# Kernel optimization log

Hardware: AMD Instinct MI355X
Metric: run time of the kernel (lower is better)

Reference implementation:

```python
import jax, jax.numpy as jnp
import numpy as np

EPS = 1e-5
K = 9  # 3x3 kernel taps


def _deform_conv_bn_relu(x, w_off, b_off, w, gamma, beta):
    B, C, H, W = x.shape
    dt = x.dtype
    # offset-predicting conv: [B, 2*K, H, W], channel layout (y,x) pairs per tap (mmcv v1)
    offset = jax.lax.conv_general_dilated(
        x, w_off, window_strides=(1, 1), padding=((1, 1), (1, 1)),
        dimension_numbers=('NCHW', 'OIHW', 'NCHW')) + b_off[None, :, None, None]
    off = offset.reshape(B, K, 2, H, W)
    # kernel tap displacements relative to output pixel (padding=1 -> centered 3x3)
    dy = (jnp.arange(K) // 3 - 1).astype(dt)
    dx = (jnp.arange(K) % 3 - 1).astype(dt)
    ii = jnp.arange(H, dtype=dt)[:, None]
    jj = jnp.arange(W, dtype=dt)[None, :]
    py = ii[None, None] + dy[None, :, None, None] + off[:, :, 0]  # [B,K,H,W]
    px = jj[None, None] + dx[None, :, None, None] + off[:, :, 1]
    y0 = jnp.floor(py)
    x0 = jnp.floor(px)
    ly = py - y0
    lx = px - x0

    xf = x.reshape(B, C, H * W)

    def gather(yc, xc, wt):
        # bilinear corner gather with zero padding outside the image
        valid = (yc >= 0) & (yc < H) & (xc >= 0) & (xc < W)
        yi = jnp.clip(yc, 0, H - 1).astype(jnp.int32)
        xi = jnp.clip(xc, 0, W - 1).astype(jnp.int32)
        idx = (yi * W + xi).reshape(B, -1)              # [B, K*H*W]
        g = jax.vmap(lambda xb, ib: xb[:, ib])(xf, idx)  # [B, C, K*H*W]
        wm = (wt * valid.astype(dt)).reshape(B, 1, -1)
        return g * wm

    val = (gather(y0, x0, (1 - ly) * (1 - lx))
           + gather(y0, x0 + 1, (1 - ly) * lx)
           + gather(y0 + 1, x0, ly * (1 - lx))
           + gather(y0 + 1, x0 + 1, ly * lx))
    val = val.reshape(B, C, K, H, W)

    # deformable conv accumulation (no bias in mmcv DeformConv2d v1)
    O = w.shape[0]
    out = jnp.einsum('ock,bckhw->bohw', w.reshape(O, C, K), val)

    # BatchNorm (training-mode batch stats) + ReLU
    mean = out.mean(axis=(0, 2, 3))
    var = out.var(axis=(0, 2, 3))
    out = (out - mean[None, :, None, None]) * jax.lax.rsqrt(var + EPS)[None, :, None, None]
    out = out * gamma[None, :, None, None] + beta[None, :, None, None]
    return jax.nn.relu(out)


def setup_inputs() -> dict:
    key = jax.random.key(0)
    k1, k2, k3 = jax.random.split(key, 3)
    B, C, O, H, W = 2, 256, 256, 128, 128
    x = jax.random.normal(k1, (B, C, H, W), dtype=jnp.float32)
    # offset branch: small init so predicted offsets stay in a realistic range
    w_off = jax.random.normal(k2, (2 * K, C, 3, 3), dtype=jnp.float32) * 0.01
    b_off = jnp.zeros((2 * K,), dtype=jnp.float32)
    w = jax.random.normal(k3, (O, C, 3, 3), dtype=jnp.float32) * 0.05
    gamma = jnp.ones((O,), dtype=jnp.float32)
    beta = jnp.zeros((O,), dtype=jnp.float32)
    return {"x": x, "w_off": w_off, "b_off": b_off, "w": w, "gamma": gamma, "beta": beta}


def reference(x, w_off, b_off, w, gamma, beta):
    return _deform_conv_bn_relu(x, w_off, b_off, w, gamma, beta)
```

## Files before the change

kernel.cpp:

```cpp
#include <hip/hip_runtime.h>
#include <hip/hip_bf16.h>

#define HWs   16384
#define Wimg  128
#define Himg  128
#define PW    130
#define PHW   16900
#define Cin   256
#define Oout  256
#define CKd   2304
#define Bb    2

typedef short   bf16x8 __attribute__((ext_vector_type(8)));
typedef float   f32x4  __attribute__((ext_vector_type(4)));

__device__ __forceinline__ float bf2f(ushort u){
  union { unsigned int i; float f; } v; v.i = ((unsigned int)u) << 16; return v.f;
}
__device__ __forceinline__ ushort f2bf(float f){
  union { float f; unsigned int i; } v; v.f = f;
  return (ushort)((v.i + 0x8000u) >> 16);
}
__device__ __forceinline__ unsigned cvt_pk_bf16(float lo, float hi){
  unsigned r;
  asm("v_cvt_pk_bf16_f32 %0, %1, %2" : "=v"(r) : "v"(lo), "v"(hi));
  return r;
}
__device__ __forceinline__ void gload_lds16(const ushort* g, void* l){
  __builtin_amdgcn_global_load_lds(
      (const __attribute__((address_space(1))) unsigned int*)g,
      (__attribute__((address_space(3))) unsigned int*)l, 16, 0, 0);
}

__global__ __launch_bounds__(256) void k_transpose(const float* __restrict__ x,
                                                   ushort* __restrict__ xtp){
  int bx = blockIdx.x;
  int b  = bx >> 10;
  int r  = bx & 1023;
  int ct = r >> 8;
  int pt = r & 255;
  int c0 = ct * 64, p0 = pt * 64;
  __shared__ float tile[64][65];
  const float* xb = x + (size_t)b * Cin * HWs;
  #pragma unroll
  for (int pass = 0; pass < 16; ++pass){
    int idx = pass * 256 + threadIdx.x;
    int cl = idx >> 6, pl = idx & 63;
    tile[cl][pl] = xb[(size_t)(c0 + cl) * HWs + p0 + pl];
  }
  __syncthreads();
  ushort* xo = xtp + (size_t)b * PHW * Cin;
  #pragma unroll
  for (int pass = 0; pass < 16; ++pass){
    int idx = pass * 256 + threadIdx.x;
    int pl = idx >> 6, cl = idx & 63;
    int hw = p0 + pl; int y = hw >> 7, xc = hw & 127;
    xo[(size_t)((y + 1) * PW + xc + 1) * Cin + c0 + cl] = f2bf(tile[cl][pl]);
  }
}

__global__ __launch_bounds__(64) void k_border(ushort* __restrict__ xtp){
  int e = blockIdx.x;
  int b = e / 516, p = e % 516;
  int y, xc;
  if (p < 130)      { y = 0;       xc = p; }
  else if (p < 260) { y = 129;     xc = p - 130; }
  else if (p < 388) { y = p - 259; xc = 0; }
  else              { y = p - 387; xc = 129; }
  uint2* dst = (uint2*)(xtp + ((size_t)b * PHW + y * PW + xc) * Cin) + threadIdx.x;
  *dst = make_uint2(0u, 0u);
}

__global__ __launch_bounds__(256) void k_wprep(const float* __restrict__ w,
                                               const float* __restrict__ wof,
                                               ushort* __restrict__ w2,
                                               ushort* __restrict__ w2of){
  int idx = blockIdx.x * 256 + threadIdx.x;
  if (idx < Oout * CKd){
    int o = idx / CKd, r = idx % CKd;
    int k = r >> 8, c = r & 255;
    w2[idx] = f2bf(w[(size_t)(o * Cin + c) * 9 + k]);
  } else {
    int j = idx - Oout * CKd;
    int o = j / CKd, r = j % CKd;
    int k = r >> 8, c = r & 255;
    float v = (o < 18) ? wof[(size_t)(o * Cin + c) * 9 + k] : 0.f;
    w2of[j] = f2bf(v);
  }
}

__global__ __launch_bounds__(512, 4) void k_offconv(const ushort* __restrict__ xtp,
                                                    const ushort* __restrict__ w2of,
                                                    const float* __restrict__ b_off,
                                                    int4* __restrict__ pidx,
                                                    float4* __restrict__ pw){
  int bx = blockIdx.x;
  int blkm = ((bx & 7) << 6) | (bx >> 3);
  int b = blkm >> 8, tile = blkm & 255;
  int hw0 = tile * 64;
  int iy = tile >> 1, jx0 = (tile & 1) * 64;
  __shared__ __align__(16) ushort aw[2][2048];
  __shared__ __align__(16) ushort bv_s[2][4096];
  __shared__ float offs_lds[18][64];
  int t = threadIdx.x, lane = t & 63, wid = t >> 6;
  int mi = wid >> 2, ni = wid & 3;
  f32x4 acc = (f32x4){0,0,0,0};
  const ushort* xb = xtp + (size_t)b * PHW * Cin;

#define OSTAGE(S, P) \
  if ((S) < 36){ int kks = (S) * 64, kt = (S) >> 2, c0s = ((S) * 64) & 255; \
    int dy = kt / 3 - 1, dxx = kt % 3 - 1; \
    if (wid < 4){ int L = t * 16; int oo = L >> 7; int inb = (L & 127) ^ ((oo & 7) << 4); \
      gload_lds16(w2of + (size_t)oo * CKd + kks + (inb >> 1), (char*)aw[P] + L); } \
    { int L = t * 16; int hw_l = L >> 7; int inb = (L & 127) ^ ((hw_l & 7) << 4); \
      int row = (iy + dy + 1) * PW + (jx0 + hw_l + dxx + 1); \
      gload_lds16(xb + (size_t)row * Cin + c0s + (inb >> 1), (char*)bv_s[P] + L); } }

  OSTAGE(0, 0);
  __syncthreads();
  #pragma unroll 1
  for (int step = 0; step < 36; ++step){
    int P = step & 1;
    OSTAGE(step + 1, P ^ 1);
    #pragma unroll
    for (int kk2 = 0; kk2 < 2; ++kk2){
      int coff = kk2 * 64 + ((lane >> 4) << 4);
      bf16x8 a0, bb;
      { int r = mi * 16 + (lane & 15); int byte = r * 128 + coff; byte ^= ((r & 7) << 4); a0 = *(const bf16x8*)((char*)aw[P] + byte); }
      { int r = ni * 16 + (lane & 15); int byte = r * 128 + coff; byte ^= ((r & 7) << 4); bb = *(const bf16x8*)((char*)bv_s[P] + byte); }
      acc = __builtin_amdgcn_mfma_f32_16x16x32_bf16(a0, bb, acc, 0, 0, 0);
    }
    __syncthreads();
  }
#undef OSTAGE
  {
    int hw_l = ni * 16 + (lane & 15);
    #pragma unroll
    for (int r = 0; r < 4; ++r){
      int o = mi * 16 + ((lane >> 4) << 2) + r;
      if (o < 18) offs_lds[o][hw_l] = acc[r] + b_off[o];
    }
  }
  __syncthreads();
  for (int idx = t; idx < 9 * 64; idx += 512){
    int k = idx >> 6, jl = idx & 63;
    int hw = hw0 + jl;
    int i = hw >> 7, jcol = hw & 127;
    float offy = offs_lds[2 * k][jl];
    float offx = offs_lds[2 * k + 1][jl];
    float py = (float)i    + (float)(k / 3 - 1) + offy;
    float px = (float)jcol + (float)(k % 3 - 1) + offx;
    float y0f = floorf(py), x0f = floorf(px);
    float ly = py - y0f, lx = px - x0f;
    int y0 = (int)y0f, x0 = (int)x0f;
    int y1 = y0 + 1, x1 = x0 + 1;
    float w00 = (1.f - ly) * (1.f - lx), w01 = (1.f - ly) * lx;
    float w10 = ly * (1.f - lx),         w11 = ly * lx;
    bool vy0 = (y0 >= 0 && y0 < 128), vy1 = (y1 >= 0 && y1 < 128);
    bool vx0 = (x0 >= 0 && x0 < 128), vx1 = (x1 >= 0 && x1 < 128);
    int iy0 = min(max(y0, 0), 127), iy1 = min(max(y1, 0), 127);
    int ix0 = min(max(x0, 0), 127), ix1 = min(max(x1, 0), 127);
    size_t e = ((size_t)b * 9 + k) * HWs + hw;
    pidx[e] = make_int4(((iy0 + 1) * PW + ix0 + 1) * Cin, ((iy0 + 1) * PW + ix1 + 1) * Cin,
                        ((iy1 + 1) * PW + ix0 + 1) * Cin, ((iy1 + 1) * PW + ix1 + 1) * Cin);
    pw[e]   = make_float4(vy0 && vx0 ? w00 : 0.f, vy0 && vx1 ? w01 : 0.f,
                          vy1 && vx0 ? w10 : 0.f, vy1 && vx1 ? w11 : 0.f);
  }
}

__device__ __forceinline__ unsigned combine_pair(unsigned d0, unsigned d1, unsigned d2, unsigned d3,
                                                 float4 wt){
  float e0 = wt.x * __uint_as_float(d0 << 16)
           + wt.y * __uint_as_float(d1 << 16)
           + wt.z * __uint_as_float(d2 << 16)
           + wt.w * __uint_as_float(d3 << 16);
  float e1 = wt.x * __uint_as_float(d0 & 0xFFFF0000u)
           + wt.y * __uint_as_float(d1 & 0xFFFF0000u)
           + wt.z * __uint_as_float(d2 & 0xFFFF0000u)
           + wt.w * __uint_as_float(d3 & 0xFFFF0000u);
  return cvt_pk_bf16(e0, e1);
}

__global__ __launch_bounds__(1024, 4) void k_main(const ushort* __restrict__ xtp,
                                                  const ushort* __restrict__ w2,
                                                  const int4* __restrict__ pidx,
                                                  const float4* __restrict__ pw,
                                                  float* __restrict__ out,
                                                  float* __restrict__ partials){
  int bx = blockIdx.x;
  int blkm = ((bx & 7) << 5) | (bx >> 3);
  int b = blkm >> 7, tile = blkm & 127;
  int hw0 = tile * 128;
  __shared__ __align__(16) ushort smem[49152];
  ushort* Ab0 = smem;
  ushort* Ab1 = smem + 16384;
  ushort* Bb0 = smem + 32768;
  ushort* Bb1 = smem + 40960;
  int t = threadIdx.x, lane = t & 63, wid = t >> 6;
  int wm = wid >> 2, wn = wid & 3;
  int cg = t & 7, hl = t >> 3;
  f32x4 acc[4][2];
  #pragma unroll
  for (int mi = 0; mi < 4; ++mi)
    #pragma unroll
    for (int ni = 0; ni < 2; ++ni) acc[mi][ni] = (f32x4){0,0,0,0};
  const ushort* xb  = xtp  + (size_t)b * PHW * Cin;
  const int4*   pib = pidx + (size_t)b * 9 * HWs + hw0;
  const float4* pwb = pw   + (size_t)b * 9 * HWs + hw0;

  int4   ids[2];
  float4 wts[2];
  uint4  g[2][4];

#define IDSLOAD(P, S) \
  if ((S) < 36){ int kq = (S) >> 2; \
    ids[P] = pib[(size_t)kq * HWs + hl]; }

#define CORNERS(P, S) \
  if ((S) < 36){ int cb = (((S) * 64) & 255) + cg * 8; int kq = (S) >> 2; \
    wts[P] = pwb[(size_t)kq * HWs + hl]; \
    g[P][0] = *(const uint4*)(xb + ids[P].x + cb); \
    g[P][1] = *(const uint4*)(xb + ids[P].y + cb); \
    g[P][2] = *(const uint4*)(xb + ids[P].z + cb); \
    g[P][3] = *(const uint4*)(xb + ids[P].w + cb); }

#define STAGEA(S, ABP) \
  if ((S) < 36){ int kks = (S) * 64; \
    _Pragma("unroll") for (int h2 = 0; h2 < 2; ++h2){ \
      int L = (wid * 2 + h2) * 1024 + lane * 16; \
      int oo = L >> 7; int inb = (L & 127) ^ ((oo & 7) << 4); \
      gload_lds16(w2 + (size_t)oo * CKd + kks + (inb >> 1), (char*)(ABP) + L); } }

#define COMBINE(P, S, BBP) \
  if ((S) < 36){ \
    float4 wtv = wts[P]; \
    uint4 ov; \
    ov.x = combine_pair(g[P][0].x, g[P][1].x, g[P][2].x, g[P][3].x, wtv); \
    ov.y = combine_pair(g[P][0].y, g[P][1].y, g[P][2].y, g[P][3].y, wtv); \
    ov.z = combine_pair(g[P][0].z, g[P][1].z, g[P][2].z, g[P][3].z, wtv); \
    ov.w = combine_pair(g[P][0].w, g[P][1].w, g[P][2].w, g[P][3].w, wtv); \
    int byte = hl * 128 + cg * 16; byte ^= ((hl & 7) << 4); \
    *(uint4*)((char*)(BBP) + byte) = ov; }

#define MFMA_PHASE(ABP, BBP) \
  { __builtin_amdgcn_s_setprio(1); \
    _Pragma("unroll") for (int kk2 = 0; kk2 < 2; ++kk2){ \
      int coff = kk2 * 64 + ((lane >> 4) << 4); \
      bf16x8 a[4], bv[2]; \
      _Pragma("unroll") for (int mi = 0; mi < 4; ++mi){ \
        int r = wm * 64 + mi * 16 + (lane & 15); \
        int byte = r * 128 + coff; byte ^= ((r & 7) << 4); \
        a[mi] = *(const bf16x8*)((const char*)(ABP) + byte); } \
      _Pragma("unroll") for (int ni = 0; ni < 2; ++ni){ \
        int r = wn * 32 + ni * 16 + (lane & 15); \
        int byte = r * 128 + coff; byte ^= ((r & 7) << 4); \
        bv[ni] = *(const bf16x8*)((const char*)(BBP) + byte); } \
      _Pragma("unroll") for (int mi = 0; mi < 4; ++mi) \
        _Pragma("unroll") for (int ni = 0; ni < 2; ++ni) \
          acc[mi][ni] = __builtin_amdgcn_mfma_f32_16x16x32_bf16(a[mi], bv[ni], acc[mi][ni], 0, 0, 0); } \
    __builtin_amdgcn_s_setprio(0); }

  IDSLOAD(0, 0);
  IDSLOAD(1, 1);
  CORNERS(0, 0);
  IDSLOAD(0, 2);
  CORNERS(1, 1);
  IDSLOAD(1, 3);
  STAGEA(0, Ab0);
  COMBINE(0, 0, Bb0);
  __syncthreads();

  #pragma unroll 1
  for (int tt = 0; tt < 36; tt += 2){
    CORNERS(0, tt + 2);
    STAGEA(tt + 1, Ab1);
    IDSLOAD(0, tt + 4);
    MFMA_PHASE(Ab0, Bb0);
    COMBINE(1, tt + 1, Bb1);
    __syncthreads();
    CORNERS(1, tt + 3);
    STAGEA(tt + 2, Ab0);
    IDSLOAD(1, tt + 5);
    MFMA_PHASE(Ab1, Bb1);
    COMBINE(0, tt + 2, Bb0);
    __syncthreads();
  }
#undef IDSLOAD
#undef CORNERS
#undef STAGEA
#undef COMBINE
#undef MFMA_PHASE

  #pragma unroll
  for (int mi = 0; mi < 4; ++mi){
    int obase = wm * 64 + mi * 16 + ((lane >> 4) << 2);
    #pragma unroll
    for (int ni = 0; ni < 2; ++ni){
      int hw = hw0 + wn * 32 + ni * 16 + (lane & 15);
      float* op = out + ((size_t)b * Oout + obase) * HWs + hw;
      #pragma unroll
      for (int r = 0; r < 4; ++r) op[(size_t)r * HWs] = acc[mi][ni][r];
    }
  }
  #pragma unroll
  for (int mi = 0; mi < 4; ++mi){
    #pragma unroll
    for (int r = 0; r < 4; ++r){
      float s = 0.f, s2 = 0.f;
      #pragma unroll
      for (int ni = 0; ni < 2; ++ni){ float v = acc[mi][ni][r]; s += v; s2 += v * v; }
      #pragma unroll
      for (int off2 = 1; off2 < 16; off2 <<= 1){
        s  += __shfl_xor(s, off2);
        s2 += __shfl_xor(s2, off2);
      }
      if ((lane & 15) == 0){
        int o = wm * 64 + mi * 16 + ((lane >> 4) << 2) + r;
        int row = blkm * 4 + wn;
        partials[(size_t)row * 256 + o] = s;
        partials[(size_t)1024 * 256 + (size_t)row * 256 + o] = s2;
      }
    }
  }
}

__global__ __launch_bounds__(256) void k_bnstats(const float* __restrict__ partials,
                                                 float* __restrict__ stats){
  int o = blockIdx.x, t = threadIdx.x;
  float s = 0.f, s2 = 0.f;
  for (int i = t; i < 1024; i += 256){
    s  += partials[(size_t)i * 256 + o];
    s2 += partials[(size_t)1024 * 256 + (size_t)i * 256 + o];
  }
  #pragma unroll
  for (int off = 32; off > 0; off >>= 1){
    s  += __shfl_down(s, off);
    s2 += __shfl_down(s2, off);
  }
  __shared__ float rs[4], rs2[4];
  int lane = t & 63, w = t >> 6;
  if (lane == 0){ rs[w] = s; rs2[w] = s2; }
  __syncthreads();
  if (t == 0){
    float S = 0.f, S2 = 0.f;
    for (int i = 0; i < 4; ++i){ S += rs[i]; S2 += rs2[i]; }
    float mean = S / 32768.f;
    float var  = S2 / 32768.f - mean * mean;
    stats[o] = mean;
    stats[256 + o] = rsqrtf(var + 1e-5f);
  }
}

__global__ __launch_bounds__(256) void k_bnapply(float* __restrict__ out,
                                                 const float* __restrict__ stats,
                                                 const float* __restrict__ gamma,
                                                 const float* __restrict__ beta){
  size_t e = ((size_t)blockIdx.x * 256 + threadIdx.x) * 4;
  int o = (int)((e >> 14) & 255);
  float mean = stats[o], rstd = stats[256 + o];
  float sc = rstd * gamma[o];
  float sh = beta[o] - mean * sc;
  float4 v = *(float4*)(out + e);
  v.x = fmaxf(v.x * sc + sh, 0.f);
  v.y = fmaxf(v.y * sc + sh, 0.f);
  v.z = fmaxf(v.z * sc + sh, 0.f);
  v.w = fmaxf(v.w * sc + sh, 0.f);
  *(float4*)(out + e) = v;
}

extern "C" void kernel_launch(void* const* d_in, const int* in_sizes, int n_in,
                              void* d_out, int out_size, void* d_ws, size_t ws_size,
                              hipStream_t stream){
  const float* x     = (const float*)d_in[0];
  const float* w_off = (const float*)d_in[1];
  const float* b_off = (const float*)d_in[2];
  const float* w     = (const float*)d_in[3];
  const float* gamma = (const float*)d_in[4];
  const float* beta  = (const float*)d_in[5];
  float* out = (float*)d_out;

  char* p = (char*)d_ws;
  ushort* xtp  = (ushort*)p; p += (size_t)Bb * PHW * Cin * 2;
  ushort* w2   = (ushort*)p; p += (size_t)Oout * CKd * 2;
  ushort* w2of = (ushort*)p; p += (size_t)32 * CKd * 2;
  int4*   pidx = (int4*)p;   p += (size_t)Bb * 9 * HWs * 16;
  float4* pwt  = (float4*)p; p += (size_t)Bb * 9 * HWs * 16;
  float*  parts= (float*)p;  p += (size_t)2 * 1024 * 256 * 4;
  float*  stats= (float*)p;

  k_transpose<<<dim3(2048), dim3(256), 0, stream>>>(x, xtp);
  k_border   <<<dim3(1032), dim3(64),  0, stream>>>(xtp);
  k_wprep    <<<dim3(2592), dim3(256), 0, stream>>>(w, w_off, w2, w2of);
  k_offconv  <<<dim3(512),  dim3(512), 0, stream>>>(xtp, w2of, b_off, pidx, pwt);
  k_main     <<<dim3(256),  dim3(1024), 0, stream>>>(xtp, w2, pidx, pwt, out, parts);
  k_bnstats  <<<dim3(256),  dim3(256), 0, stream>>>(parts, stats);
  k_bnapply  <<<dim3(8192), dim3(256), 0, stream>>>(out, stats, gamma, beta);
}
```

Measured before the change: 125.4 us.

## Load weight fragments directly into registers instead of staging through LDS

The weight (A) operand is no longer staged into LDS via global_load_lds. Each wave now loads its bf16 fragments straight from global memory into registers, double-buffered across k-halves, which cuts LDS use from 96KB to 32KB. The corner gather pipeline is reduced to a single register set, and barriers become a manual s_waitcnt vmcnt(5) plus s_barrier so loads stay in flight across the barrier. The cost is redundant global/L2 traffic for weights across the four wn waves, and a risk that the hand-written waitcnt count is wrong.

```diff
diff --git a/kernel.cpp b/kernel.cpp
--- a/kernel.cpp
+++ b/kernel.cpp
@@ -14,9 +14,6 @@
 typedef short   bf16x8 __attribute__((ext_vector_type(8)));
 typedef float   f32x4  __attribute__((ext_vector_type(4)));
 
-__device__ __forceinline__ float bf2f(ushort u){
-  union { unsigned int i; float f; } v; v.i = ((unsigned int)u) << 16; return v.f;
-}
 __device__ __forceinline__ ushort f2bf(float f){
   union { float f; unsigned int i; } v; v.f = f;
   return (ushort)((v.i + 0x8000u) >> 16);
@@ -191,11 +188,8 @@
   int blkm = ((bx & 7) << 5) | (bx >> 3);
   int b = blkm >> 7, tile = blkm & 127;
   int hw0 = tile * 128;
-  __shared__ __align__(16) ushort smem[49152];
-  ushort* Ab0 = smem;
-  ushort* Ab1 = smem + 16384;
-  ushort* Bb0 = smem + 32768;
-  ushort* Bb1 = smem + 40960;
+  __shared__ __align__(16) ushort Bb0[8192];
+  __shared__ __align__(16) ushort Bb1[8192];
   int t = threadIdx.x, lane = t & 63, wid = t >> 6;
   int wm = wid >> 2, wn = wid & 3;
   int cg = t & 7, hl = t >> 3;
@@ -207,89 +201,92 @@
   const ushort* xb  = xtp  + (size_t)b * PHW * Cin;
   const int4*   pib = pidx + (size_t)b * 9 * HWs + hw0;
   const float4* pwb = pw   + (size_t)b * 9 * HWs + hw0;
-
-  int4   ids[2];
-  float4 wts[2];
-  uint4  g[2][4];
-
-#define IDSLOAD(P, S) \
-  if ((S) < 36){ int kq = (S) >> 2; \
-    ids[P] = pib[(size_t)kq * HWs + hl]; }
-
-#define CORNERS(P, S) \
-  if ((S) < 36){ int cb = (((S) * 64) & 255) + cg * 8; int kq = (S) >> 2; \
-    wts[P] = pwb[(size_t)kq * HWs + hl]; \
-    g[P][0] = *(const uint4*)(xb + ids[P].x + cb); \
-    g[P][1] = *(const uint4*)(xb + ids[P].y + cb); \
-    g[P][2] = *(const uint4*)(xb + ids[P].z + cb); \
-    g[P][3] = *(const uint4*)(xb + ids[P].w + cb); }
-
-#define STAGEA(S, ABP) \
-  if ((S) < 36){ int kks = (S) * 64; \
-    _Pragma("unroll") for (int h2 = 0; h2 < 2; ++h2){ \
-      int L = (wid * 2 + h2) * 1024 + lane * 16; \
-      int oo = L >> 7; int inb = (L & 127) ^ ((oo & 7) << 4); \
-      gload_lds16(w2 + (size_t)oo * CKd + kks + (inb >> 1), (char*)(ABP) + L); } }
-
-#define COMBINE(P, S, BBP) \
-  if ((S) < 36){ \
-    float4 wtv = wts[P]; \
-    uint4 ov; \
-    ov.x = combine_pair(g[P][0].x, g[P][1].x, g[P][2].x, g[P][3].x, wtv); \
-    ov.y = combine_pair(g[P][0].y, g[P][1].y, g[P][2].y, g[P][3].y, wtv); \
-    ov.z = combine_pair(g[P][0].z, g[P][1].z, g[P][2].z, g[P][3].z, wtv); \
-    ov.w = combine_pair(g[P][0].w, g[P][1].w, g[P][2].w, g[P][3].w, wtv); \
+  const ushort* w2t = w2 + (size_t)(wm * 64 + (lane & 15)) * CKd + ((lane >> 4) << 3);
+
+  int4   ids0, ids1;
+  float4 wtc;
+  uint4  g[4];
+  bf16x8 a0[4], a1[4];
+
+#define PIPE_BARRIER() do { \
+    asm volatile("s_waitcnt vmcnt(5) lgkmcnt(0)" ::: "memory"); \
+    __builtin_amdgcn_sched_barrier(0); \
+    __builtin_amdgcn_s_barrier(); \
+    __builtin_amdgcn_sched_barrier(0); \
+  } while (0)
+
+#define IDSLOAD(DST, S) \
+  { int kq = ((S) < 36 ? (S) : 35) >> 2; DST = pib[(size_t)kq * HWs + hl]; }
+
+#define CORNERS(IDS, S) \
+  { int Sc = ((S) < 36 ? (S) : 35); \
+    int cb = ((Sc * 64) & 255) + cg * 8; int kq = Sc >> 2; \
+    wtc = pwb[(size_t)kq * HWs + hl]; \
+    g[0] = *(const uint4*)(xb + IDS.x + cb); \
+    g[1] = *(const uint4*)(xb + IDS.y + cb); \
+    g[2] = *(const uint4*)(xb + IDS.z + cb); \
+    g[3] = *(const uint4*)(xb + IDS.w + cb); }
+
+#define ALOAD(A, S, KK2) \
+  { int kks = ((S) < 36 ? (S) : 35) * 64 + (KK2) * 32; \
+    _Pragma("unroll") for (int mi = 0; mi < 4; ++mi) \
+      A[mi] = *(const bf16x8*)(w2t + (size_t)mi * 16 * CKd + kks); }
+
+#define COMBINE(BBP) \
+  { uint4 ov; \
+    ov.x = combine_pair(g[0].x, g[1].x, g[2].x, g[3].x, wtc); \
+    ov.y = combine_pair(g[0].y, g[1].y, g[2].y, g[3].y, wtc); \
+    ov.z = combine_pair(g[0].z, g[1].z, g[2].z, g[3].z, wtc); \
+    ov.w = combine_pair(g[0].w, g[1].w, g[2].w, g[3].w, wtc); \
     int byte = hl * 128 + cg * 16; byte ^= ((hl & 7) << 4); \
     *(uint4*)((char*)(BBP) + byte) = ov; }
 
-#define MFMA_PHASE(ABP, BBP) \
-  { __builtin_amdgcn_s_setprio(1); \
-    _Pragma("unroll") for (int kk2 = 0; kk2 < 2; ++kk2){ \
-      int coff = kk2 * 64 + ((lane >> 4) << 4); \
-      bf16x8 a[4], bv[2]; \
-      _Pragma("unroll") for (int mi = 0; mi < 4; ++mi){ \
-        int r = wm * 64 + mi * 16 + (lane & 15); \
-        int byte = r * 128 + coff; byte ^= ((r & 7) << 4); \
-        a[mi] = *(const bf16x8*)((const char*)(ABP) + byte); } \
-      _Pragma("unroll") for (int ni = 0; ni < 2; ++ni){ \
-        int r = wn * 32 + ni * 16 + (lane & 15); \
-        int byte = r * 128 + coff; byte ^= ((r & 7) << 4); \
-        bv[ni] = *(const bf16x8*)((const char*)(BBP) + byte); } \
-      _Pragma("unroll") for (int mi = 0; mi < 4; ++mi) \
-        _Pragma("unroll") for (int ni = 0; ni < 2; ++ni) \
-          acc[mi][ni] = __builtin_amdgcn_mfma_f32_16x16x32_bf16(a[mi], bv[ni], acc[mi][ni], 0, 0, 0); } \
+#define MFMA_K(A, KK2, BBP) \
+  { int coff = (KK2) * 64 + ((lane >> 4) << 4); \
+    bf16x8 bv[2]; \
+    _Pragma("unroll") for (int ni = 0; ni < 2; ++ni){ \
+      int r = wn * 32 + ni * 16 + (lane & 15); \
+      int byte = r * 128 + coff; byte ^= ((r & 7) << 4); \
+      bv[ni] = *(const bf16x8*)((const char*)(BBP) + byte); } \
+    __builtin_amdgcn_s_setprio(1); \
+    _Pragma("unroll") for (int mi = 0; mi < 4; ++mi) \
+      _Pragma("unroll") for (int ni = 0; ni < 2; ++ni) \
+        acc[mi][ni] = __builtin_amdgcn_mfma_f32_16x16x32_bf16(A[mi], bv[ni], acc[mi][ni], 0, 0, 0); \
     __builtin_amdgcn_s_setprio(0); }
 
-  IDSLOAD(0, 0);
-  IDSLOAD(1, 1);
-  CORNERS(0, 0);
-  IDSLOAD(0, 2);
-  CORNERS(1, 1);
-  IDSLOAD(1, 3);
-  STAGEA(0, Ab0);
-  COMBINE(0, 0, Bb0);
-  __syncthreads();
+  IDSLOAD(ids0, 0);
+  IDSLOAD(ids1, 1);
+  CORNERS(ids0, 0);
+  ALOAD(a0, 0, 0);
+  COMBINE(Bb0);
+  IDSLOAD(ids0, 2);
+  PIPE_BARRIER();
 
   #pragma unroll 1
   for (int tt = 0; tt < 36; tt += 2){
-    CORNERS(0, tt + 2);
-    STAGEA(tt + 1, Ab1);
-    IDSLOAD(0, tt + 4);
-    MFMA_PHASE(Ab0, Bb0);
-    COMBINE(1, tt + 1, Bb1);
-    __syncthreads();
-    CORNERS(1, tt + 3);
-    STAGEA(tt + 2, Ab0);
-    IDSLOAD(1, tt + 5);
-    MFMA_PHASE(Ab1, Bb1);
-    COMBINE(0, tt + 2, Bb0);
-    __syncthreads();
-  }
+    CORNERS(ids1, tt + 1);
+    IDSLOAD(ids1, tt + 3);
+    ALOAD(a1, tt, 1);
+    MFMA_K(a0, 0, Bb0);
+    ALOAD(a0, tt + 1, 0);
+    MFMA_K(a1, 1, Bb0);
+    COMBINE(Bb1);
+    PIPE_BARRIER();
+    CORNERS(ids0, tt + 2);
+    IDSLOAD(ids0, tt + 4);
+    ALOAD(a1, tt + 1, 1);
+    MFMA_K(a0, 0, Bb1);
+    ALOAD(a0, tt + 2, 0);
+    MFMA_K(a1, 1, Bb1);
+    COMBINE(Bb0);
+    PIPE_BARRIER();
+  }
+#undef PIPE_BARRIER
 #undef IDSLOAD
 #undef CORNERS
-#undef STAGEA
+#undef ALOAD
 #undef COMBINE
-#undef MFMA_PHASE
+#undef MFMA_K
 
   #pragma unroll
   for (int mi = 0; mi < 4; ++mi){
```

Measured after the change: 230.2 us. 1.84x slower.

## Build bilinear B fragments in registers and drop the LDS B buffer

Applied to the files above, without the earlier changes.

The main deformable-conv GEMM kernel now uses 8 waves instead of 16, each computing 128 output channels by 32 pixels. Each lane gathers its bilinear corners and combines them straight into MFMA B-operand registers, so the LDS staging of the sampled B tile is gone and only the weight A tile is double-buffered. The goal is to cut LDS traffic and the B write/read round trip. In exchange, each wave reissues the gathers (every pixel is gathered once per wm wave), the accumulators double, occupancy falls, and gather latency is less hidden across the synchronisation barrier.

```diff
diff --git a/kernel.cpp b/kernel.cpp
--- a/kernel.cpp
+++ b/kernel.cpp
@@ -14,9 +14,6 @@
 typedef short   bf16x8 __attribute__((ext_vector_type(8)));
 typedef float   f32x4  __attribute__((ext_vector_type(4)));
 
-__device__ __forceinline__ float bf2f(ushort u){
-  union { unsigned int i; float f; } v; v.i = ((unsigned int)u) << 16; return v.f;
-}
 __device__ __forceinline__ ushort f2bf(float f){
   union { float f; unsigned int i; } v; v.f = f;
   return (ushort)((v.i + 0x8000u) >> 16);
@@ -181,141 +178,140 @@
   return cvt_pk_bf16(e0, e1);
 }
 
-__global__ __launch_bounds__(1024, 4) void k_main(const ushort* __restrict__ xtp,
-                                                  const ushort* __restrict__ w2,
-                                                  const int4* __restrict__ pidx,
-                                                  const float4* __restrict__ pw,
-                                                  float* __restrict__ out,
-                                                  float* __restrict__ partials){
+__global__ __launch_bounds__(512, 2) void k_main(const ushort* __restrict__ xtp,
+                                                 const ushort* __restrict__ w2,
+                                                 const int4* __restrict__ pidx,
+                                                 const float4* __restrict__ pw,
+                                                 float* __restrict__ out,
+                                                 float* __restrict__ partials){
   int bx = blockIdx.x;
   int blkm = ((bx & 7) << 5) | (bx >> 3);
   int b = blkm >> 7, tile = blkm & 127;
   int hw0 = tile * 128;
-  __shared__ __align__(16) ushort smem[49152];
-  ushort* Ab0 = smem;
-  ushort* Ab1 = smem + 16384;
-  ushort* Bb0 = smem + 32768;
-  ushort* Bb1 = smem + 40960;
+  __shared__ __align__(16) ushort Ab0[16384];
+  __shared__ __align__(16) ushort Ab1[16384];
   int t = threadIdx.x, lane = t & 63, wid = t >> 6;
   int wm = wid >> 2, wn = wid & 3;
-  int cg = t & 7, hl = t >> 3;
-  f32x4 acc[4][2];
-  #pragma unroll
-  for (int mi = 0; mi < 4; ++mi)
-    #pragma unroll
-    for (int ni = 0; ni < 2; ++ni) acc[mi][ni] = (f32x4){0,0,0,0};
+  int pix0 = wn * 32 + (lane & 15);
+  int chsub = (lane >> 4) << 3;
+  f32x4 acc[8][2];
+  #pragma unroll
+  for (int mi = 0; mi < 8; ++mi)
+    #pragma unroll
+    for (int nj = 0; nj < 2; ++nj) acc[mi][nj] = (f32x4){0,0,0,0};
   const ushort* xb  = xtp  + (size_t)b * PHW * Cin;
   const int4*   pib = pidx + (size_t)b * 9 * HWs + hw0;
   const float4* pwb = pw   + (size_t)b * 9 * HWs + hw0;
 
-  int4   ids[2];
-  float4 wts[2];
+  int4   idc0, idc1;
+  float4 wtc0, wtc1;
   uint4  g[2][4];
-
-#define IDSLOAD(P, S) \
-  if ((S) < 36){ int kq = (S) >> 2; \
-    ids[P] = pib[(size_t)kq * HWs + hl]; }
-
-#define CORNERS(P, S) \
-  if ((S) < 36){ int cb = (((S) * 64) & 255) + cg * 8; int kq = (S) >> 2; \
-    wts[P] = pwb[(size_t)kq * HWs + hl]; \
-    g[P][0] = *(const uint4*)(xb + ids[P].x + cb); \
-    g[P][1] = *(const uint4*)(xb + ids[P].y + cb); \
-    g[P][2] = *(const uint4*)(xb + ids[P].z + cb); \
-    g[P][3] = *(const uint4*)(xb + ids[P].w + cb); }
+  bf16x8 a[4], a2[4];
+  bf16x8 bf[2];
 
 #define STAGEA(S, ABP) \
-  if ((S) < 36){ int kks = (S) * 64; \
-    _Pragma("unroll") for (int h2 = 0; h2 < 2; ++h2){ \
-      int L = (wid * 2 + h2) * 1024 + lane * 16; \
+  { int kks = ((S) < 36 ? (S) : 35) * 64; \
+    _Pragma("unroll") for (int h2 = 0; h2 < 4; ++h2){ \
+      int L = (wid * 4 + h2) * 1024 + lane * 16; \
       int oo = L >> 7; int inb = (L & 127) ^ ((oo & 7) << 4); \
       gload_lds16(w2 + (size_t)oo * CKd + kks + (inb >> 1), (char*)(ABP) + L); } }
 
-#define COMBINE(P, S, BBP) \
-  if ((S) < 36){ \
-    float4 wtv = wts[P]; \
-    uint4 ov; \
-    ov.x = combine_pair(g[P][0].x, g[P][1].x, g[P][2].x, g[P][3].x, wtv); \
-    ov.y = combine_pair(g[P][0].y, g[P][1].y, g[P][2].y, g[P][3].y, wtv); \
-    ov.z = combine_pair(g[P][0].z, g[P][1].z, g[P][2].z, g[P][3].z, wtv); \
-    ov.w = combine_pair(g[P][0].w, g[P][1].w, g[P][2].w, g[P][3].w, wtv); \
-    int byte = hl * 128 + cg * 16; byte ^= ((hl & 7) << 4); \
-    *(uint4*)((char*)(BBP) + byte) = ov; }
-
-#define MFMA_PHASE(ABP, BBP) \
-  { __builtin_amdgcn_s_setprio(1); \
-    _Pragma("unroll") for (int kk2 = 0; kk2 < 2; ++kk2){ \
-      int coff = kk2 * 64 + ((lane >> 4) << 4); \
-      bf16x8 a[4], bv[2]; \
-      _Pragma("unroll") for (int mi = 0; mi < 4; ++mi){ \
-        int r = wm * 64 + mi * 16 + (lane & 15); \
-        int byte = r * 128 + coff; byte ^= ((r & 7) << 4); \
-        a[mi] = *(const bf16x8*)((const char*)(ABP) + byte); } \
-      _Pragma("unroll") for (int ni = 0; ni < 2; ++ni){ \
-        int r = wn * 32 + ni * 16 + (lane & 15); \
-        int byte = r * 128 + coff; byte ^= ((r & 7) << 4); \
-        bv[ni] = *(const bf16x8*)((const char*)(BBP) + byte); } \
-      _Pragma("unroll") for (int mi = 0; mi < 4; ++mi) \
-        _Pragma("unroll") for (int ni = 0; ni < 2; ++ni) \
-          acc[mi][ni] = __builtin_amdgcn_mfma_f32_16x16x32_bf16(a[mi], bv[ni], acc[mi][ni], 0, 0, 0); } \
-    __builtin_amdgcn_s_setprio(0); }
-
-  IDSLOAD(0, 0);
-  IDSLOAD(1, 1);
-  CORNERS(0, 0);
-  IDSLOAD(0, 2);
-  CORNERS(1, 1);
-  IDSLOAD(1, 3);
+#define CLOAD(KK2, C0) \
+  { int cbl = (C0) + (KK2) * 32 + chsub; \
+    g[0][0] = *(const uint4*)(xb + idc0.x + cbl); \
+    g[0][1] = *(const uint4*)(xb + idc0.y + cbl); \
+    g[0][2] = *(const uint4*)(xb + idc0.z + cbl); \
+    g[0][3] = *(const uint4*)(xb + idc0.w + cbl); \
+    g[1][0] = *(const uint4*)(xb + idc1.x + cbl); \
+    g[1][1] = *(const uint4*)(xb + idc1.y + cbl); \
+    g[1][2] = *(const uint4*)(xb + idc1.z + cbl); \
+    g[1][3] = *(const uint4*)(xb + idc1.w + cbl); }
+
+#define BCOMB() \
+  { union { uint4 u; bf16x8 v; } r0, r1; \
+    r0.u.x = combine_pair(g[0][0].x, g[0][1].x, g[0][2].x, g[0][3].x, wtc0); \
+    r0.u.y = combine_pair(g[0][0].y, g[0][1].y, g[0][2].y, g[0][3].y, wtc0); \
+    r0.u.z = combine_pair(g[0][0].z, g[0][1].z, g[0][2].z, g[0][3].z, wtc0); \
+    r0.u.w = combine_pair(g[0][0].w, g[0][1].w, g[0][2].w, g[0][3].w, wtc0); \
+    r1.u.x = combine_pair(g[1][0].x, g[1][1].x, g[1][2].x, g[1][3].x, wtc1); \
+    r1.u.y = combine_pair(g[1][0].y, g[1][1].y, g[1][2].y, g[1][3].y, wtc1); \
+    r1.u.z = combine_pair(g[1][0].z, g[1][1].z, g[1][2].z, g[1][3].z, wtc1); \
+    r1.u.w = combine_pair(g[1][0].w, g[1][1].w, g[1][2].w, g[1][3].w, wtc1); \
+    bf[0] = r0.v; bf[1] = r1.v; }
+
+#define AREAD(DST, KK2, MI0, ABP) \
+  { _Pragma("unroll") for (int q = 0; q < 4; ++q){ \
+      int row = wm * 128 + ((MI0) + q) * 16 + (lane & 15); \
+      int byte = row * 128 + (KK2) * 64 + ((lane >> 4) << 4); byte ^= ((row & 7) << 4); \
+      DST[q] = *(const bf16x8*)((const char*)(ABP) + byte); } }
+
+#define MFMA8(A4, MI0) \
+  { _Pragma("unroll") for (int q = 0; q < 4; ++q) \
+      _Pragma("unroll") for (int nj = 0; nj < 2; ++nj) \
+        acc[(MI0) + q][nj] = __builtin_amdgcn_mfma_f32_16x16x32_bf16(A4[q], bf[nj], acc[(MI0) + q][nj], 0, 0, 0); }
+
   STAGEA(0, Ab0);
-  COMBINE(0, 0, Bb0);
   __syncthreads();
 
   #pragma unroll 1
-  for (int tt = 0; tt < 36; tt += 2){
-    CORNERS(0, tt + 2);
-    STAGEA(tt + 1, Ab1);
-    IDSLOAD(0, tt + 4);
-    MFMA_PHASE(Ab0, Bb0);
-    COMBINE(1, tt + 1, Bb1);
-    __syncthreads();
-    CORNERS(1, tt + 3);
-    STAGEA(tt + 2, Ab0);
-    IDSLOAD(1, tt + 5);
-    MFMA_PHASE(Ab1, Bb1);
-    COMBINE(0, tt + 2, Bb0);
-    __syncthreads();
-  }
-#undef IDSLOAD
-#undef CORNERS
+  for (int tap = 0; tap < 9; ++tap){
+    idc0 = pib[(size_t)tap * HWs + pix0];
+    idc1 = pib[(size_t)tap * HWs + pix0 + 16];
+    wtc0 = pwb[(size_t)tap * HWs + pix0];
+    wtc1 = pwb[(size_t)tap * HWs + pix0 + 16];
+    #pragma unroll
+    for (int sub = 0; sub < 4; ++sub){
+      const int P = tap * 4 + sub;
+      const int c0 = sub * 64;
+      ushort* Acur = (sub & 1) ? Ab1 : Ab0;
+      ushort* Anxt = (sub & 1) ? Ab0 : Ab1;
+      CLOAD(0, c0);
+      STAGEA(P + 1, Anxt);
+      AREAD(a,  0, 0, Acur);
+      AREAD(a2, 0, 4, Acur);
+      BCOMB();
+      MFMA8(a, 0);
+      CLOAD(1, c0);
+      MFMA8(a2, 4);
+      AREAD(a,  1, 0, Acur);
+      AREAD(a2, 1, 4, Acur);
+      BCOMB();
+      MFMA8(a, 0);
+      MFMA8(a2, 4);
+      __syncthreads();
+    }
+  }
 #undef STAGEA
-#undef COMBINE
-#undef MFMA_PHASE
-
-  #pragma unroll
-  for (int mi = 0; mi < 4; ++mi){
-    int obase = wm * 64 + mi * 16 + ((lane >> 4) << 2);
-    #pragma unroll
-    for (int ni = 0; ni < 2; ++ni){
-      int hw = hw0 + wn * 32 + ni * 16 + (lane & 15);
+#undef CLOAD
+#undef BCOMB
+#undef AREAD
+#undef MFMA8
+
+  #pragma unroll
+  for (int mi = 0; mi < 8; ++mi){
+    int obase = wm * 128 + mi * 16 + ((lane >> 4) << 2);
+    #pragma unroll
+    for (int nj = 0; nj < 2; ++nj){
+      int hw = hw0 + wn * 32 + nj * 16 + (lane & 15);
       float* op = out + ((size_t)b * Oout + obase) * HWs + hw;
       #pragma unroll
-      for (int r = 0; r < 4; ++r) op[(size_t)r * HWs] = acc[mi][ni][r];
-    }
-  }
-  #pragma unroll
-  for (int mi = 0; mi < 4; ++mi){
+      for (int r = 0; r < 4; ++r) op[(size_t)r * HWs] = acc[mi][nj][r];
+    }
+  }
+  #pragma unroll
+  for (int mi = 0; mi < 8; ++mi){
     #pragma unroll
     for (int r = 0; r < 4; ++r){
       float s = 0.f, s2 = 0.f;
       #pragma unroll
-      for (int ni = 0; ni < 2; ++ni){ float v = acc[mi][ni][r]; s += v; s2 += v * v; }
+      for (int nj = 0; nj < 2; ++nj){ float v = acc[mi][nj][r]; s += v; s2 += v * v; }
       #pragma unroll
       for (int off2 = 1; off2 < 16; off2 <<= 1){
         s  += __shfl_xor(s, off2);
         s2 += __shfl_xor(s2, off2);
       }
       if ((lane & 15) == 0){
-        int o = wm * 64 + mi * 16 + ((lane >> 4) << 2) + r;
+        int o = wm * 128 + mi * 16 + ((lane >> 4) << 2) + r;
         int row = blkm * 4 + wn;
         partials[(size_t)row * 256 + o] = s;
         partials[(size_t)1024 * 256 + (size_t)row * 256 + o] = s2;
@@ -392,7 +388,7 @@
   k_border   <<<dim3(1032), dim3(64),  0, stream>>>(xtp);
   k_wprep    <<<dim3(2592), dim3(256), 0, stream>>>(w, w_off, w2, w2of);
   k_offconv  <<<dim3(512),  dim3(512), 0, stream>>>(xtp, w2of, b_off, pidx, pwt);
-  k_main     <<<dim3(256),  dim3(1024), 0, stream>>>(xtp, w2, pidx, pwt, out, parts);
+  k_main     <<<dim3(256),  dim3(512), 0, stream>>>(xtp, w2, pidx, pwt, out, parts);
   k_bnstats  <<<dim3(256),  dim3(256), 0, stream>>>(parts, stats);
   k_bnapply  <<<dim3(8192), dim3(256), 0, stream>>>(out, stats, gamma, beta);
 }
```

Measured after the change: 242.2 us. 1.93x slower.

## Store pre-BN conv output as bf16 and factor bilinear weights separably

Applied to the files above, without the earlier changes.

The main kernel writes its pre-normalization output to a bf16 scratch buffer, and a new BN-apply kernel reads bf16 and writes the fp32 result. This halves the intermediate write and read traffic. The offset kernel now stores separable y/x bilinear weights, and the corner combine interpolates along x and then y using packed float2 math. BN statistics are still computed from the fp32 accumulators, but rounding the stored activations to bf16 adds error, and the fast path only runs if the workspace is large enough.

```diff
diff --git a/kernel.cpp b/kernel.cpp
--- a/kernel.cpp
+++ b/kernel.cpp
@@ -13,10 +13,8 @@
 
 typedef short   bf16x8 __attribute__((ext_vector_type(8)));
 typedef float   f32x4  __attribute__((ext_vector_type(4)));
-
-__device__ __forceinline__ float bf2f(ushort u){
-  union { unsigned int i; float f; } v; v.i = ((unsigned int)u) << 16; return v.f;
-}
+typedef float   f32x2  __attribute__((ext_vector_type(2)));
+
 __device__ __forceinline__ ushort f2bf(float f){
   union { float f; unsigned int i; } v; v.f = f;
   return (ushort)((v.i + 0x8000u) >> 16);
@@ -154,8 +152,6 @@
     float ly = py - y0f, lx = px - x0f;
     int y0 = (int)y0f, x0 = (int)x0f;
     int y1 = y0 + 1, x1 = x0 + 1;
-    float w00 = (1.f - ly) * (1.f - lx), w01 = (1.f - ly) * lx;
-    float w10 = ly * (1.f - lx),         w11 = ly * lx;
     bool vy0 = (y0 >= 0 && y0 < 128), vy1 = (y1 >= 0 && y1 < 128);
     bool vx0 = (x0 >= 0 && x0 < 128), vx1 = (x1 >= 0 && x1 < 128);
     int iy0 = min(max(y0, 0), 127), iy1 = min(max(y1, 0), 127);
@@ -163,29 +159,28 @@
     size_t e = ((size_t)b * 9 + k) * HWs + hw;
     pidx[e] = make_int4(((iy0 + 1) * PW + ix0 + 1) * Cin, ((iy0 + 1) * PW + ix1 + 1) * Cin,
                         ((iy1 + 1) * PW + ix0 + 1) * Cin, ((iy1 + 1) * PW + ix1 + 1) * Cin);
-    pw[e]   = make_float4(vy0 && vx0 ? w00 : 0.f, vy0 && vx1 ? w01 : 0.f,
-                          vy1 && vx0 ? w10 : 0.f, vy1 && vx1 ? w11 : 0.f);
-  }
-}
-
-__device__ __forceinline__ unsigned combine_pair(unsigned d0, unsigned d1, unsigned d2, unsigned d3,
+    pw[e]   = make_float4(vy0 ? (1.f - ly) : 0.f, vy1 ? ly : 0.f,
+                          vx0 ? (1.f - lx) : 0.f, vx1 ? lx : 0.f);
+  }
+}
+
+__device__ __forceinline__ f32x2 up2(unsigned d){
+  f32x2 r; r.x = __uint_as_float(d << 16); r.y = __uint_as_float(d & 0xFFFF0000u); return r;
+}
+__device__ __forceinline__ unsigned combine_pair(unsigned d00, unsigned d01, unsigned d10, unsigned d11,
                                                  float4 wt){
-  float e0 = wt.x * __uint_as_float(d0 << 16)
-           + wt.y * __uint_as_float(d1 << 16)
-           + wt.z * __uint_as_float(d2 << 16)
-           + wt.w * __uint_as_float(d3 << 16);
-  float e1 = wt.x * __uint_as_float(d0 & 0xFFFF0000u)
-           + wt.y * __uint_as_float(d1 & 0xFFFF0000u)
-           + wt.z * __uint_as_float(d2 & 0xFFFF0000u)
-           + wt.w * __uint_as_float(d3 & 0xFFFF0000u);
-  return cvt_pk_bf16(e0, e1);
-}
-
+  f32x2 t0 = wt.z * up2(d00) + wt.w * up2(d01);
+  f32x2 t1 = wt.z * up2(d10) + wt.w * up2(d11);
+  f32x2 e  = wt.x * t0 + wt.y * t1;
+  return cvt_pk_bf16(e.x, e.y);
+}
+
+template<int BF16OUT>
 __global__ __launch_bounds__(1024, 4) void k_main(const ushort* __restrict__ xtp,
                                                   const ushort* __restrict__ w2,
                                                   const int4* __restrict__ pidx,
                                                   const float4* __restrict__ pw,
-                                                  float* __restrict__ out,
+                                                  void* __restrict__ outp,
                                                   float* __restrict__ partials){
   int bx = blockIdx.x;
   int blkm = ((bx & 7) << 5) | (bx >> 3);
@@ -297,9 +292,15 @@
     #pragma unroll
     for (int ni = 0; ni < 2; ++ni){
       int hw = hw0 + wn * 32 + ni * 16 + (lane & 15);
-      float* op = out + ((size_t)b * Oout + obase) * HWs + hw;
-      #pragma unroll
-      for (int r = 0; r < 4; ++r) op[(size_t)r * HWs] = acc[mi][ni][r];
+      if (BF16OUT){
+        ushort* ob = (ushort*)outp + ((size_t)b * Oout + obase) * HWs + hw;
+        #pragma unroll
+        for (int r = 0; r < 4; ++r) ob[(size_t)r * HWs] = f2bf(acc[mi][ni][r]);
+      } else {
+        float* op = (float*)outp + ((size_t)b * Oout + obase) * HWs + hw;
+        #pragma unroll
+        for (int r = 0; r < 4; ++r) op[(size_t)r * HWs] = acc[mi][ni][r];
+      }
     }
   }
   #pragma unroll
@@ -368,6 +369,30 @@
   *(float4*)(out + e) = v;
 }
 
+__global__ __launch_bounds__(256) void k_bnapply_b(const ushort* __restrict__ outb,
+                                                   float* __restrict__ out,
+                                                   const float* __restrict__ stats,
+                                                   const float* __restrict__ gamma,
+                                                   const float* __restrict__ beta){
+  size_t e = ((size_t)blockIdx.x * 256 + threadIdx.x) * 8;
+  int o = (int)((e >> 14) & 255);
+  float mean = stats[o], rstd = stats[256 + o];
+  float sc = rstd * gamma[o];
+  float sh = beta[o] - mean * sc;
+  uint4 v = *(const uint4*)(outb + e);
+  float4 r0, r1;
+  r0.x = fmaxf(__uint_as_float(v.x << 16)          * sc + sh, 0.f);
+  r0.y = fmaxf(__uint_as_float(v.x & 0xFFFF0000u)  * sc + sh, 0.f);
+  r0.z = fmaxf(__uint_as_float(v.y << 16)          * sc + sh, 0.f);
+  r0.w = fmaxf(__uint_as_float(v.y & 0xFFFF0000u)  * sc + sh, 0.f);
+  r1.x = fmaxf(__uint_as_float(v.z << 16)          * sc + sh, 0.f);
+  r1.y = fmaxf(__uint_as_float(v.z & 0xFFFF0000u)  * sc + sh, 0.f);
+  r1.z = fmaxf(__uint_as_float(v.w << 16)          * sc + sh, 0.f);
+  r1.w = fmaxf(__uint_as_float(v.w & 0xFFFF0000u)  * sc + sh, 0.f);
+  *(float4*)(out + e)     = r0;
+  *(float4*)(out + e + 4) = r1;
+}
+
 extern "C" void kernel_launch(void* const* d_in, const int* in_sizes, int n_in,
                               void* d_out, int out_size, void* d_ws, size_t ws_size,
                               hipStream_t stream){
@@ -386,13 +411,21 @@
   int4*   pidx = (int4*)p;   p += (size_t)Bb * 9 * HWs * 16;
   float4* pwt  = (float4*)p; p += (size_t)Bb * 9 * HWs * 16;
   float*  parts= (float*)p;  p += (size_t)2 * 1024 * 256 * 4;
-  float*  stats= (float*)p;
+  float*  stats= (float*)p;  p += 4096;
+  ushort* outb = (ushort*)p; p += (size_t)Bb * Oout * HWs * 2;
+  size_t need = (size_t)(p - (char*)d_ws);
 
   k_transpose<<<dim3(2048), dim3(256), 0, stream>>>(x, xtp);
   k_border   <<<dim3(1032), dim3(64),  0, stream>>>(xtp);
   k_wprep    <<<dim3(2592), dim3(256), 0, stream>>>(w, w_off, w2, w2of);
   k_offconv  <<<dim3(512),  dim3(512), 0, stream>>>(xtp, w2of, b_off, pidx, pwt);
-  k_main     <<<dim3(256),  dim3(1024), 0, stream>>>(xtp, w2, pidx, pwt, out, parts);
-  k_bnstats  <<<dim3(256),  dim3(256), 0, stream>>>(parts, stats);
-  k_bnapply  <<<dim3(8192), dim3(256), 0, stream>>>(out, stats, gamma, beta);
-}
+  if (ws_size >= need){
+    k_main<1>  <<<dim3(256),  dim3(1024), 0, stream>>>(xtp, w2, pidx, pwt, (void*)outb, parts);
+    k_bnstats  <<<dim3(256),  dim3(256), 0, stream>>>(parts, stats);
+    k_bnapply_b<<<dim3(4096), dim3(256), 0, stream>>>(outb, out, stats, gamma, beta);
+  } else {
+    k_main<0>  <<<dim3(256),  dim3(1024), 0, stream>>>(xtp, w2, pidx, pwt, (void*)out, parts);
+    k_bnstats  <<<dim3(256),  dim3(256), 0, stream>>>(parts, stats);
+    k_bnapply  <<<dim3(8192), dim3(256), 0, stream>>>(out, stats, gamma, beta);
+  }
+}
```

Measured after the change: 125.1 us. No clear change (-0.2%).
